# Optimization experiments

Hardware: AMD Instinct MI355X
Metric: run time of the kernel (lower is better)

Reference implementation:

```python
import jax, jax.numpy as jnp
import numpy as np
import math

NUM_HEADS = 16
D_MODEL = 1024
D_HEAD = D_MODEL // NUM_HEADS
B, S = 2, 2048


def setup_inputs() -> dict:
    key = jax.random.key(0)
    k1, k2 = jax.random.split(key)
    query = jax.random.normal(k1, (B, S, D_MODEL), dtype=jnp.float32)
    # causal mask: True where masked (j > i)
    mask = jnp.broadcast_to(jnp.triu(jnp.ones((S, S), dtype=bool), k=1), (B, S, S))
    W_o = jax.random.normal(k2, (D_MODEL, D_MODEL), dtype=jnp.float32) * (1.0 / math.sqrt(D_MODEL))
    b_o = jnp.zeros((D_MODEL,), dtype=jnp.float32)
    return {"query": query, "mask": mask, "W_o": W_o, "b_o": b_o}


def reference(query, mask, W_o, b_o):
    # NOTE: faithful to source — q/k/v linear layers are never applied in forward.
    # Self-attention: key = value = query.
    Bq, Sq, D = query.shape
    # split heads: [B, S, D] -> [B, H, S, dh]
    q = query.reshape(Bq, Sq, NUM_HEADS, D_HEAD).transpose(0, 2, 1, 3)
    k = q
    v = q
    # logits: [B, H, Sq, Sk]
    logits = jnp.einsum("bhqd,bhkd->bhqk", q, k) / math.sqrt(D_HEAD)
    logits = jnp.where(mask[:, None, :, :], -jnp.inf, logits)
    attn = jax.nn.softmax(logits, axis=-1)          # [B, H, Sq, Sk]
    out = jnp.einsum("bhqk,bhkd->bhqd", attn, v)    # [B, H, Sq, dh]
    # merge heads: [B, Sq, D]
    out = out.transpose(0, 2, 1, 3).reshape(Bq, Sq, D)
    # output projection (torch Linear: x @ W.T + b)
    return out @ W_o.T + b_o
```

## Files before the change

kernel.cpp:

```cpp
#include <hip/hip_runtime.h>
#include <hip/hip_bf16.h>
#include <stdint.h>

#define SEQ 2048
#define DMODEL 1024

typedef __attribute__((ext_vector_type(8))) short short8;
typedef __attribute__((ext_vector_type(4))) float floatx4;

__device__ __forceinline__ floatx4 mfma16x16x32(short8 a, short8 b, floatx4 c) {
  return __builtin_amdgcn_mfma_f32_16x16x32_bf16(a, b, c, 0, 0, 0);
}

__device__ __forceinline__ uint16_t f2bf(float x) {
  __hip_bfloat16 h = __float2bfloat16(x);
  return *reinterpret_cast<uint16_t*>(&h);
}

__device__ __forceinline__ float bf2f(uint16_t u) {
  uint32_t x = (uint32_t)u << 16;
  union { uint32_t u; float f; } c; c.u = x; return c.f;
}

__device__ __forceinline__ void glds16(const uint16_t* g, uint16_t* l) {
  __builtin_amdgcn_global_load_lds(
      (const __attribute__((address_space(1))) uint32_t*)g,
      (__attribute__((address_space(3))) uint32_t*)(uint32_t)(uintptr_t)l,
      16, 0, 0);
}

__global__ __launch_bounds__(256) void cvt_kernel(
    const float* __restrict__ q, uint16_t* __restrict__ qd,
    const float* __restrict__ w, uint16_t* __restrict__ wd,
    int nq4, int ntot4) {
  int i = blockIdx.x * 256 + threadIdx.x;
  if (i >= ntot4) return;
  const float* src = (i < nq4) ? q : w;
  uint16_t* dst = (i < nq4) ? qd : wd;
  int j = (i < nq4) ? i : i - nq4;
  float4 v = ((const float4*)src)[j];
  ushort4 r;
  r.x = f2bf(v.x); r.y = f2bf(v.y); r.z = f2bf(v.z); r.w = f2bf(v.w);
  ((ushort4*)dst)[j] = r;
}

__device__ __forceinline__ int vt_idx(int d, int key) {
  return d * 64 + ((((key >> 3) ^ (d >> 3) ^ d) & 7) << 3) + (key & 7);
}

__device__ __forceinline__ int ps_idx(int row, int col) {
  return row * 64 + ((((col >> 3) ^ row) & 7) << 3) + (col & 7);
}

__global__ __launch_bounds__(256, 2) void attn_kernel(
    const uint16_t* __restrict__ qbf, uint16_t* __restrict__ Opart,
    float* __restrict__ Lpart) {
  const int w    = blockIdx.x >> 5;
  const int qt   = 15 - (w >> 1);
  const int half = w & 1;
  const int bh   = blockIdx.x & 31;
  const int b    = bh >> 4;
  const int h    = bh & 15;
  const int tid  = threadIdx.x;
  const int wave = tid >> 6;
  const int lane = tid & 63;
  const int l15  = lane & 15;
  const int quad = lane >> 4;

  __shared__ uint16_t Vt[2][64 * 64];
  __shared__ uint16_t Ps[4][2][16 * 64];

  const uint16_t* base = qbf + (size_t)b * SEQ * DMODEL + h * 64;

  short8 qf[2][2];
  #pragma unroll
  for (int s = 0; s < 2; ++s)
    #pragma unroll
    for (int ks = 0; ks < 2; ++ks)
      qf[s][ks] = *(const short8*)(base +
          (size_t)(qt * 128 + s * 64 + wave * 16 + l15) * DMODEL + ks * 32 + quad * 8);

  floatx4 o_acc[2][4];
  float l_run[2][4];
  #pragma unroll
  for (int s = 0; s < 2; ++s) {
    #pragma unroll
    for (int dt = 0; dt < 4; ++dt) o_acc[s][dt] = (floatx4){0.f, 0.f, 0.f, 0.f};
    #pragma unroll
    for (int r = 0; r < 4; ++r) l_run[s][r] = 0.f;
  }

  const int r0 = tid >> 3;
  const int cg = (tid & 7) * 8;

  auto stage = [&](int kt, int buf) {
    uint4 v0 = *(const uint4*)(base + (size_t)(kt * 64 + r0) * DMODEL + cg);
    uint4 v1 = *(const uint4*)(base + (size_t)(kt * 64 + 32 + r0) * DMODEL + cg);
    uint16_t t0[8], t1[8];
    *(uint4*)t0 = v0;
    *(uint4*)t1 = v1;
    #pragma unroll
    for (int i = 0; i < 8; ++i) Vt[buf][vt_idx(cg + i, r0)] = t0[i];
    #pragma unroll
    for (int i = 0; i < 8; ++i) Vt[buf][vt_idx(cg + i, 32 + r0)] = t1[i];
  };

  const int ktlo = half ? (qt + 1) : 0;
  const int kthi = half ? (2 * qt + 1) : qt;
  stage(ktlo, ktlo & 1);

  auto iter = [&](int kt, int nt0, int nt1, bool d0, bool d1, int ks0m, int ks1m) {
    __syncthreads();
    if (kt < kthi) stage(kt + 1, (kt + 1) & 1);
    const int buf = kt & 1;

    floatx4 sacc[2][4];
    #pragma unroll
    for (int s = 0; s < 2; ++s)
      #pragma unroll
      for (int nt = 0; nt < 4; ++nt) sacc[s][nt] = (floatx4){0.f, 0.f, 0.f, 0.f};

    #pragma unroll
    for (int ks = 0; ks < 2; ++ks)
      #pragma unroll
      for (int nt = 0; nt < 4; ++nt) {
        short8 kf = *(const short8*)(base +
            (size_t)(kt * 64 + nt * 16 + l15) * DMODEL + ks * 32 + quad * 8);
        if (nt <= nt0) sacc[0][nt] = mfma16x16x32(qf[0][ks], kf, sacc[0][nt]);
        if (nt <= nt1) sacc[1][nt] = mfma16x16x32(qf[1][ks], kf, sacc[1][nt]);
      }

    #pragma unroll
    for (int s = 0; s < 2; ++s) {
      const int ntm = s ? nt1 : nt0;
      const bool dg = s ? d1 : d0;
      const int ksm = s ? ks1m : ks0m;
      if (ntm < 0) continue;
      uint16_t* Pw = Ps[wave][s];
      #pragma unroll
      for (int nt = 0; nt < 4; ++nt) {
        const int lcol = nt * 16 + l15;
        if (nt <= ntm) {
          #pragma unroll
          for (int r = 0; r < 4; ++r) {
            float p = __builtin_amdgcn_exp2f(fmaf(sacc[s][nt][r], 0.1803369f, -10.f));
            if (dg && nt == wave && l15 > quad * 4 + r) p = 0.f;
            l_run[s][r] += p;
            Pw[ps_idx(quad * 4 + r, lcol)] = f2bf(p);
          }
        } else if (nt <= 2 * ksm + 1) {
          #pragma unroll
          for (int r = 0; r < 4; ++r) Pw[ps_idx(quad * 4 + r, lcol)] = 0;
        }
      }
      #pragma unroll
      for (int ks = 0; ks < 2; ++ks)
        if (ks <= ksm) {
          short8 pf = *(const short8*)&Pw[ps_idx(l15, ks * 32 + quad * 8)];
          #pragma unroll
          for (int dt = 0; dt < 4; ++dt) {
            short8 vf = *(const short8*)&Vt[buf][vt_idx(dt * 16 + l15, ks * 32 + quad * 8)];
            o_acc[s][dt] = mfma16x16x32(pf, vf, o_acc[s][dt]);
          }
        }
    }
  };

  const int kdiag = (wave < 2) ? 0 : 1;
  if (half == 0) {
    if (qt == 0) {
      iter(0, wave, 3, true, false, kdiag, 1);
    } else {
      for (int kt = 0; kt <= qt; ++kt) iter(kt, 3, 3, false, false, 1, 1);
    }
  } else {
    for (int kt = qt + 1; kt < 2 * qt; ++kt) iter(kt, 3, 3, false, false, 1, 1);
    if (qt >= 1) iter(2 * qt, wave, 3, true, false, kdiag, 1);
    iter(2 * qt + 1, -1, wave, false, true, 0, kdiag);
  }

  const size_t obase = (size_t)half * (4096 * 1024);
  #pragma unroll
  for (int s = 0; s < 2; ++s)
    #pragma unroll
    for (int r = 0; r < 4; ++r) {
      float l = l_run[s][r];
      #pragma unroll
      for (int off = 1; off < 16; off <<= 1) l += __shfl_xor(l, off, 64);
      int rowg = b * SEQ + qt * 128 + s * 64 + wave * 16 + quad * 4 + r;
      if (l15 == 0) Lpart[half * 65536 + h * 4096 + rowg] = l;
      #pragma unroll
      for (int dt = 0; dt < 4; ++dt)
        Opart[obase + (size_t)rowg * DMODEL + h * 64 + dt * 16 + l15] =
            f2bf(o_acc[s][dt][r]);
    }
}

__global__ __launch_bounds__(256) void combine_kernel(
    const uint16_t* __restrict__ Opart, const float* __restrict__ Lpart,
    uint16_t* __restrict__ X) {
  int i = blockIdx.x * 256 + threadIdx.x;
  int row = i >> 7;
  int c8  = (i & 127) * 8;
  int h   = c8 >> 6;
  float inv = 1.0f / (Lpart[h * 4096 + row] + Lpart[65536 + h * 4096 + row]);
  uint16_t a[8], bpt[8], o[8];
  *(uint4*)a   = *(const uint4*)&Opart[(size_t)row * DMODEL + c8];
  *(uint4*)bpt = *(const uint4*)&Opart[(size_t)4096 * 1024 + (size_t)row * DMODEL + c8];
  #pragma unroll
  for (int k = 0; k < 8; ++k)
    o[k] = f2bf((bf2f(a[k]) + bf2f(bpt[k])) * inv);
  *(uint4*)&X[(size_t)row * DMODEL + c8] = *(uint4*)o;
}

__global__ __launch_bounds__(256, 4) void proj_kernel(
    const uint16_t* __restrict__ X, const uint16_t* __restrict__ Wo,
    const float* __restrict__ bo, float* __restrict__ out) {
  const int bx = blockIdx.x;
  const int by = blockIdx.y;
  const int tid = threadIdx.x;
  const int wave = tid >> 6, lane = tid & 63, l15 = lane & 15, quad = lane >> 4;
  const int wr = wave >> 1, wc = wave & 1;

  __shared__ uint16_t As[2][128 * 32];
  __shared__ uint16_t Bs[2][64 * 32];

  floatx4 acc[4][2];
  #pragma unroll
  for (int mt = 0; mt < 4; ++mt)
    #pragma unroll
    for (int nt = 0; nt < 2; ++nt) acc[mt][nt] = (floatx4){0.f, 0.f, 0.f, 0.f};

  const int rw = lane >> 2;
  const int kp = 8 * ((lane & 3) ^ ((lane >> 2) & 3));

  auto stage = [&](int kt, int buf) {
    glds16(X + (size_t)(bx * 128 + wave * 16 + rw) * DMODEL + kt * 32 + kp,
           &As[buf][(wave * 16) * 32 + lane * 8]);
    glds16(X + (size_t)(bx * 128 + 64 + wave * 16 + rw) * DMODEL + kt * 32 + kp,
           &As[buf][(64 + wave * 16) * 32 + lane * 8]);
    glds16(Wo + (size_t)(by * 64 + wave * 16 + rw) * DMODEL + kt * 32 + kp,
           &Bs[buf][(wave * 16) * 32 + lane * 8]);
  };

  stage(0, 0);
  for (int kt = 0; kt < 32; ++kt) {
    __syncthreads();
    if (kt < 31) stage(kt + 1, (kt + 1) & 1);
    const int buf = kt & 1;
    short8 af[4], bf2[2];
    #pragma unroll
    for (int mt = 0; mt < 4; ++mt) {
      int row = wr * 64 + mt * 16 + l15;
      af[mt] = *(const short8*)&As[buf][row * 32 + ((quad ^ (row & 3)) << 3)];
    }
    #pragma unroll
    for (int nt = 0; nt < 2; ++nt) {
      int row = wc * 32 + nt * 16 + l15;
      bf2[nt] = *(const short8*)&Bs[buf][row * 32 + ((quad ^ (row & 3)) << 3)];
    }
    #pragma unroll
    for (int mt = 0; mt < 4; ++mt)
      #pragma unroll
      for (int nt = 0; nt < 2; ++nt)
        acc[mt][nt] = mfma16x16x32(af[mt], bf2[nt], acc[mt][nt]);
  }

  #pragma unroll
  for (int nt = 0; nt < 2; ++nt) {
    int colg = by * 64 + wc * 32 + nt * 16 + l15;
    float bias = bo[colg];
    #pragma unroll
    for (int mt = 0; mt < 4; ++mt)
      #pragma unroll
      for (int r2 = 0; r2 < 4; ++r2) {
        int rowg = bx * 128 + wr * 64 + mt * 16 + quad * 4 + r2;
        out[(size_t)rowg * DMODEL + colg] = acc[mt][nt][r2] + bias;
      }
  }
}

extern "C" void kernel_launch(void* const* d_in, const int* in_sizes, int n_in,
                              void* d_out, int out_size, void* d_ws, size_t ws_size,
                              hipStream_t stream) {
  const float* q_f32  = (const float*)d_in[0];
  const float* Wo_f32 = (const float*)d_in[2];
  const float* bo     = (const float*)d_in[3];
  float* out = (float*)d_out;

  uint16_t* qbf   = (uint16_t*)d_ws;
  uint16_t* X     = (uint16_t*)((char*)d_ws + (size_t)8 * 1024 * 1024);
  uint16_t* wobf  = (uint16_t*)((char*)d_ws + (size_t)16 * 1024 * 1024);
  uint16_t* Opart = (uint16_t*)((char*)d_ws + (size_t)18 * 1024 * 1024);
  float*    Lpart = (float*)((char*)d_ws + (size_t)34 * 1024 * 1024);

  const int nq4 = 2 * SEQ * DMODEL / 4;
  const int nw4 = DMODEL * DMODEL / 4;
  const int nt4 = nq4 + nw4;
  cvt_kernel<<<dim3((nt4 + 255) / 256), dim3(256), 0, stream>>>(
      q_f32, qbf, Wo_f32, wobf, nq4, nt4);

  attn_kernel<<<dim3(1024), dim3(256), 0, stream>>>(qbf, Opart, Lpart);
  combine_kernel<<<dim3(2048), dim3(256), 0, stream>>>(Opart, Lpart, X);
  proj_kernel<<<dim3(32, 16), dim3(256), 0, stream>>>(X, wobf, bo, out);
}
```

Baseline: 163.0 us.

## Keep P in registers by computing transposed S and using 16x16x16 MFMA for PV

Swaps the QK^T MFMA operands so each lane holds S^T values laid out as the A-operand of a 16x16x16 bf16 MFMA. The P matrix then feeds the PV product straight from registers instead of going through a per-wave shared-memory round trip. V staging is changed to pack two keys per 32-bit LDS store, the row-sum reduction is simplified, and K loads are skipped for fully masked tiles. In exchange, the PV product now uses twice as many smaller MFMAs.

```diff
diff --git a/kernel.cpp b/kernel.cpp
--- a/kernel.cpp
+++ b/kernel.cpp
@@ -6,10 +6,15 @@
 #define DMODEL 1024
 
 typedef __attribute__((ext_vector_type(8))) short short8;
+typedef __attribute__((ext_vector_type(4))) short short4v;
 typedef __attribute__((ext_vector_type(4))) float floatx4;
 
 __device__ __forceinline__ floatx4 mfma16x16x32(short8 a, short8 b, floatx4 c) {
   return __builtin_amdgcn_mfma_f32_16x16x32_bf16(a, b, c, 0, 0, 0);
+}
+
+__device__ __forceinline__ floatx4 mfma16x16x16(short4v a, short4v b, floatx4 c) {
+  return __builtin_amdgcn_mfma_f32_16x16x16bf16_1k(a, b, c, 0, 0, 0);
 }
 
 __device__ __forceinline__ uint16_t f2bf(float x) {
@@ -46,10 +51,6 @@
 
 __device__ __forceinline__ int vt_idx(int d, int key) {
   return d * 64 + ((((key >> 3) ^ (d >> 3) ^ d) & 7) << 3) + (key & 7);
-}
-
-__device__ __forceinline__ int ps_idx(int row, int col) {
-  return row * 64 + ((((col >> 3) ^ row) & 7) << 3) + (col & 7);
 }
 
 __global__ __launch_bounds__(256, 2) void attn_kernel(
@@ -68,7 +69,6 @@
   const int quad = lane >> 4;
 
   __shared__ uint16_t Vt[2][64 * 64];
-  __shared__ uint16_t Ps[4][2][16 * 64];
 
   const uint16_t* base = qbf + (size_t)b * SEQ * DMODEL + h * 64;
 
@@ -81,35 +81,35 @@
           (size_t)(qt * 128 + s * 64 + wave * 16 + l15) * DMODEL + ks * 32 + quad * 8);
 
   floatx4 o_acc[2][4];
-  float l_run[2][4];
+  float l_run[2];
   #pragma unroll
   for (int s = 0; s < 2; ++s) {
     #pragma unroll
     for (int dt = 0; dt < 4; ++dt) o_acc[s][dt] = (floatx4){0.f, 0.f, 0.f, 0.f};
-    #pragma unroll
-    for (int r = 0; r < 4; ++r) l_run[s][r] = 0.f;
+    l_run[s] = 0.f;
   }
 
   const int r0 = tid >> 3;
   const int cg = (tid & 7) * 8;
 
   auto stage = [&](int kt, int buf) {
-    uint4 v0 = *(const uint4*)(base + (size_t)(kt * 64 + r0) * DMODEL + cg);
-    uint4 v1 = *(const uint4*)(base + (size_t)(kt * 64 + 32 + r0) * DMODEL + cg);
+    uint4 v0 = *(const uint4*)(base + (size_t)(kt * 64 + 2 * r0) * DMODEL + cg);
+    uint4 v1 = *(const uint4*)(base + (size_t)(kt * 64 + 2 * r0 + 1) * DMODEL + cg);
     uint16_t t0[8], t1[8];
     *(uint4*)t0 = v0;
     *(uint4*)t1 = v1;
     #pragma unroll
-    for (int i = 0; i < 8; ++i) Vt[buf][vt_idx(cg + i, r0)] = t0[i];
-    #pragma unroll
-    for (int i = 0; i < 8; ++i) Vt[buf][vt_idx(cg + i, 32 + r0)] = t1[i];
+    for (int i = 0; i < 8; ++i) {
+      uint32_t pk = (uint32_t)t0[i] | ((uint32_t)t1[i] << 16);
+      *(uint32_t*)&Vt[buf][vt_idx(cg + i, 2 * r0)] = pk;
+    }
   };
 
   const int ktlo = half ? (qt + 1) : 0;
   const int kthi = half ? (2 * qt + 1) : qt;
   stage(ktlo, ktlo & 1);
 
-  auto iter = [&](int kt, int nt0, int nt1, bool d0, bool d1, int ks0m, int ks1m) {
+  auto iter = [&](int kt, int nt0, int nt1, bool d0, bool d1) {
     __syncthreads();
     if (kt < kthi) stage(kt + 1, (kt + 1) & 1);
     const int buf = kt & 1;
@@ -124,76 +124,69 @@
     for (int ks = 0; ks < 2; ++ks)
       #pragma unroll
       for (int nt = 0; nt < 4; ++nt) {
+        if (nt > nt0 && nt > nt1) continue;
         short8 kf = *(const short8*)(base +
             (size_t)(kt * 64 + nt * 16 + l15) * DMODEL + ks * 32 + quad * 8);
-        if (nt <= nt0) sacc[0][nt] = mfma16x16x32(qf[0][ks], kf, sacc[0][nt]);
-        if (nt <= nt1) sacc[1][nt] = mfma16x16x32(qf[1][ks], kf, sacc[1][nt]);
-      }
-
-    #pragma unroll
-    for (int s = 0; s < 2; ++s) {
-      const int ntm = s ? nt1 : nt0;
-      const bool dg = s ? d1 : d0;
-      const int ksm = s ? ks1m : ks0m;
-      if (ntm < 0) continue;
-      uint16_t* Pw = Ps[wave][s];
-      #pragma unroll
-      for (int nt = 0; nt < 4; ++nt) {
-        const int lcol = nt * 16 + l15;
-        if (nt <= ntm) {
-          #pragma unroll
-          for (int r = 0; r < 4; ++r) {
-            float p = __builtin_amdgcn_exp2f(fmaf(sacc[s][nt][r], 0.1803369f, -10.f));
-            if (dg && nt == wave && l15 > quad * 4 + r) p = 0.f;
-            l_run[s][r] += p;
-            Pw[ps_idx(quad * 4 + r, lcol)] = f2bf(p);
-          }
-        } else if (nt <= 2 * ksm + 1) {
-          #pragma unroll
-          for (int r = 0; r < 4; ++r) Pw[ps_idx(quad * 4 + r, lcol)] = 0;
+        if (nt <= nt0) sacc[0][nt] = mfma16x16x32(kf, qf[0][ks], sacc[0][nt]);
+        if (nt <= nt1) sacc[1][nt] = mfma16x16x32(kf, qf[1][ks], sacc[1][nt]);
+      }
+
+    #pragma unroll
+    for (int nt = 0; nt < 4; ++nt) {
+      if (nt > nt0 && nt > nt1) continue;
+      short4v vf[4];
+      #pragma unroll
+      for (int dt = 0; dt < 4; ++dt)
+        vf[dt] = *(const short4v*)&Vt[buf][vt_idx(dt * 16 + l15, nt * 16 + quad * 4)];
+      #pragma unroll
+      for (int s = 0; s < 2; ++s) {
+        const int ntm = s ? nt1 : nt0;
+        const bool dg = s ? d1 : d0;
+        if (nt > ntm) continue;
+        short4v pf;
+        #pragma unroll
+        for (int r = 0; r < 4; ++r) {
+          float p = __builtin_amdgcn_exp2f(fmaf(sacc[s][nt][r], 0.1803369f, -10.f));
+          if (dg && nt == wave && quad * 4 + r > l15) p = 0.f;
+          l_run[s] += p;
+          pf[r] = (short)f2bf(p);
         }
-      }
-      #pragma unroll
-      for (int ks = 0; ks < 2; ++ks)
-        if (ks <= ksm) {
-          short8 pf = *(const short8*)&Pw[ps_idx(l15, ks * 32 + quad * 8)];
-          #pragma unroll
-          for (int dt = 0; dt < 4; ++dt) {
-            short8 vf = *(const short8*)&Vt[buf][vt_idx(dt * 16 + l15, ks * 32 + quad * 8)];
-            o_acc[s][dt] = mfma16x16x32(pf, vf, o_acc[s][dt]);
-          }
-        }
+        #pragma unroll
+        for (int dt = 0; dt < 4; ++dt)
+          o_acc[s][dt] = mfma16x16x16(pf, vf[dt], o_acc[s][dt]);
+      }
     }
   };
 
-  const int kdiag = (wave < 2) ? 0 : 1;
   if (half == 0) {
     if (qt == 0) {
-      iter(0, wave, 3, true, false, kdiag, 1);
+      iter(0, wave, 3, true, false);
     } else {
-      for (int kt = 0; kt <= qt; ++kt) iter(kt, 3, 3, false, false, 1, 1);
+      for (int kt = 0; kt <= qt; ++kt) iter(kt, 3, 3, false, false);
     }
   } else {
-    for (int kt = qt + 1; kt < 2 * qt; ++kt) iter(kt, 3, 3, false, false, 1, 1);
-    if (qt >= 1) iter(2 * qt, wave, 3, true, false, kdiag, 1);
-    iter(2 * qt + 1, -1, wave, false, true, 0, kdiag);
+    for (int kt = qt + 1; kt < 2 * qt; ++kt) iter(kt, 3, 3, false, false);
+    if (qt >= 1) iter(2 * qt, wave, 3, true, false);
+    iter(2 * qt + 1, -1, wave, false, true);
   }
 
   const size_t obase = (size_t)half * (4096 * 1024);
   #pragma unroll
-  for (int s = 0; s < 2; ++s)
-    #pragma unroll
-    for (int r = 0; r < 4; ++r) {
-      float l = l_run[s][r];
-      #pragma unroll
-      for (int off = 1; off < 16; off <<= 1) l += __shfl_xor(l, off, 64);
-      int rowg = b * SEQ + qt * 128 + s * 64 + wave * 16 + quad * 4 + r;
-      if (l15 == 0) Lpart[half * 65536 + h * 4096 + rowg] = l;
-      #pragma unroll
-      for (int dt = 0; dt < 4; ++dt)
-        Opart[obase + (size_t)rowg * DMODEL + h * 64 + dt * 16 + l15] =
+  for (int s = 0; s < 2; ++s) {
+    float l = l_run[s];
+    l += __shfl_xor(l, 16, 64);
+    l += __shfl_xor(l, 32, 64);
+    int rowg = b * SEQ + qt * 128 + s * 64 + wave * 16 + l15;
+    if (quad == 0) Lpart[half * 65536 + h * 4096 + rowg] = l;
+    #pragma unroll
+    for (int dt = 0; dt < 4; ++dt)
+      #pragma unroll
+      for (int r = 0; r < 4; ++r) {
+        int rowo = b * SEQ + qt * 128 + s * 64 + wave * 16 + quad * 4 + r;
+        Opart[obase + (size_t)rowo * DMODEL + h * 64 + dt * 16 + l15] =
             f2bf(o_acc[s][dt][r]);
-    }
+      }
+  }
 }
 
 __global__ __launch_bounds__(256) void combine_kernel(
```

After: 156.1 us. 4.2% less time.
